# Performance work log

Hardware: AMD Instinct MI355X
Metric: run time of the kernel (lower is better)

Reference implementation:

```python
import jax, jax.numpy as jnp
import numpy as np

TAU = 0.3
EPS = 1e-8
B, N = 16, 65536


def _box2gaussian(boxes):
    # boxes: (B, N, 7) = (cx, cy, cz, dx, dy, dz, theta)
    mu = boxes[..., :3]
    dxyz = boxes[..., 3:6]
    theta = boxes[..., 6]
    c, s = jnp.cos(theta), jnp.sin(theta)
    z, o = jnp.zeros_like(c), jnp.ones_like(c)
    # Rz: (B, N, 3, 3) rotation about z
    Rz = jnp.stack([
        jnp.stack([c, -s, z], axis=-1),
        jnp.stack([s,  c, z], axis=-1),
        jnp.stack([z,  z, o], axis=-1),
    ], axis=-2)
    diag = dxyz ** 2 / 4.0                       # (B, N, 3)
    # sigma = Rz @ diag(diag) @ Rz^T
    sigma = jnp.einsum('bnij,bnj,bnkj->bnik', Rz, diag, Rz)
    return mu, sigma


def _sqrtm_psd(A):
    # Batched symmetric matrix square root via eigendecomposition.
    # Faithful to torch.linalg.eig + clamp(real, 1e-8) + V diag(sqrt(w)) V^T
    # for symmetric PSD input (eig of symmetric == eigh).
    A = 0.5 * (A + jnp.swapaxes(A, -1, -2))      # symmetrize for robustness
    w, v = jnp.linalg.eigh(A)
    w = jnp.clip(w, EPS, None)
    return jnp.einsum('...ij,...j,...kj->...ik', v, jnp.sqrt(w), v)


def setup_inputs() -> dict:
    key = jax.random.key(0)
    k1, k2 = jax.random.split(key)
    pred = jax.random.normal(k1, (B, N, 7), dtype=jnp.float32)
    gt = jax.random.normal(k2, (B, N, 7), dtype=jnp.float32)
    return {"pred_bboxes_3d": pred, "gt_bboxes_3d": gt}


def reference(pred_bboxes_3d, gt_bboxes_3d):
    mu_p, sigma_p = _box2gaussian(pred_bboxes_3d)
    mu_t, sigma_t = _box2gaussian(gt_bboxes_3d)

    # ||mu_p - mu_t||^2, (B, N)
    mu_dist_sq = jnp.sum((mu_p - mu_t) ** 2, axis=-1)

    # Tr(Sp + St - 2 (Sp^1/2 St Sp^1/2)^1/2), vectorized over all B*N boxes
    sp_sqrt = _sqrtm_psd(sigma_p)
    spstsp = sp_sqrt @ sigma_t @ sp_sqrt
    spstsp_sqrt = _sqrtm_psd(spstsp)
    cov_term = jnp.trace(sigma_p + sigma_t - 2.0 * spstsp_sqrt,
                         axis1=-2, axis2=-1)

    w2_sq = mu_dist_sq + cov_term

    det_sigma_t = jnp.clip(jnp.linalg.det(sigma_t), EPS, None)
    det_term = det_sigma_t ** (1.0 / 3.0)
    loss_per_box = 1.0 - jnp.exp(-w2_sq / (TAU * det_term))

    valid_mask = (gt_bboxes_3d[..., 0] != 0).astype(loss_per_box.dtype)
    loss = (loss_per_box * valid_mask).sum() / (valid_mask.sum() + EPS)
    return loss
```

## Files before the change

kernel.cpp:

```cpp
#include <hip/hip_runtime.h>
#include <math.h>

#define TAU_F 0.3f
#define EPS_F 1e-8f

__global__ void gwd_kernel(const float* __restrict__ pred,
                           const float* __restrict__ gt,
                           float* __restrict__ sums, int n) {
    float acc_loss = 0.f, acc_mask = 0.f;
    const int stride = gridDim.x * blockDim.x;
    for (int i = blockIdx.x * blockDim.x + threadIdx.x; i < n; i += stride) {
        const float* p = pred + (size_t)i * 7;
        const float* g = gt   + (size_t)i * 7;
        float px = p[0], py = p[1], pz = p[2];
        float pdx = p[3], pdy = p[4], pdz = p[5], pth = p[6];
        float tx = g[0], ty = g[1], tz = g[2];
        float tdx = g[3], tdy = g[4], tdz = g[5], tth = g[6];

        float dx = px - tx, dy = py - ty, dz = pz - tz;
        float mu_dist = dx * dx + dy * dy + dz * dz;

        float ap1 = 0.25f * pdx * pdx, ap2 = 0.25f * pdy * pdy, czp = 0.25f * pdz * pdz;
        float at1 = 0.25f * tdx * tdx, at2 = 0.25f * tdy * tdy, czt = 0.25f * tdz * tdz;

        float sp, cp; sincosf(pth, &sp, &cp);
        float st, ct; sincosf(tth, &st, &ct);
        float cp2 = cp * cp, sp2 = sp * sp, cpsp = cp * sp;
        float ct2 = ct * ct, st2 = st * st, ctst = ct * st;

        float At11 = at1 * ct2 + at2 * st2;
        float At22 = at1 * st2 + at2 * ct2;
        float At12 = (at1 - at2) * ctst;

        float ap1c = fmaxf(ap1, EPS_F), ap2c = fmaxf(ap2, EPS_F);
        float Ap11 = ap1c * cp2 + ap2c * sp2;
        float Ap22 = ap1c * sp2 + ap2c * cp2;
        float Ap12 = (ap1c - ap2c) * cpsp;

        float T = At11 * Ap11 + 2.f * At12 * Ap12 + At22 * Ap22;
        float D = (at1 * at2) * (ap1c * ap2c);
        float r = sqrtf(fmaxf(T * T - 4.f * D, 0.f));
        float lm1 = 0.5f * (T + r), lm2 = 0.5f * (T - r);
        float tr_sqrt_M2 = sqrtf(fmaxf(lm1, EPS_F)) + sqrtf(fmaxf(lm2, EPS_F));

        float czpc = fmaxf(czp, EPS_F);
        float z_sqrt = sqrtf(fmaxf(czpc * czt, EPS_F));

        float cov = (ap1 + ap2 + czp) + (at1 + at2 + czt)
                    - 2.f * (tr_sqrt_M2 + z_sqrt);
        float w2 = mu_dist + cov;

        float det_t = fmaxf(at1 * at2 * czt, EPS_F);
        float det_term = cbrtf(det_t);
        float loss = 1.f - expf(-w2 / (TAU_F * det_term));
        float mask = (tx != 0.f) ? 1.f : 0.f;
        acc_loss += loss * mask;
        acc_mask += mask;
    }

    for (int off = 32; off; off >>= 1) {
        acc_loss += __shfl_down(acc_loss, off, 64);
        acc_mask += __shfl_down(acc_mask, off, 64);
    }
    __shared__ float sl[8], sm[8];
    int lane = threadIdx.x & 63, wave = threadIdx.x >> 6;
    if (lane == 0) { sl[wave] = acc_loss; sm[wave] = acc_mask; }
    __syncthreads();
    if (threadIdx.x == 0) {
        float tl = 0.f, tm = 0.f;
        int nw = blockDim.x >> 6;
        for (int w = 0; w < nw; ++w) { tl += sl[w]; tm += sm[w]; }
        atomicAdd(&sums[0], tl);
        atomicAdd(&sums[1], tm);
    }
}

__global__ void gwd_finalize(const float* __restrict__ sums,
                             float* __restrict__ out) {
    if (threadIdx.x == 0 && blockIdx.x == 0) {
        out[0] = sums[0] / (sums[1] + EPS_F);
    }
}

extern "C" void kernel_launch(void* const* d_in, const int* in_sizes, int n_in,
                              void* d_out, int out_size, void* d_ws, size_t ws_size,
                              hipStream_t stream) {
    const float* pred = (const float*)d_in[0];
    const float* gt   = (const float*)d_in[1];
    float* out  = (float*)d_out;
    float* sums = (float*)d_ws;
    int n = in_sizes[0] / 7;

    hipMemsetAsync(sums, 0, 2 * sizeof(float), stream);

    const int block = 256;
    const int grid  = 1024;
    gwd_kernel<<<grid, block, 0, stream>>>(pred, gt, sums, n);
    gwd_finalize<<<1, 64, 0, stream>>>(sums, out);
}
```

Baseline: 113.7 us.

## Vectorize per-thread box loads and replace atomics with partial-sum finalize

Each thread now handles exactly four boxes, reading them as seven contiguous float4 nontemporal loads per input instead of strided scalar loads in a grid-stride loop. The per-block atomicAdds and the memset are replaced by per-block partial sums written to workspace, reduced by a 1024-thread finalize kernel. The aim is wider, better-used memory transactions and less launch and atomic overhead. Grid and block sizes are hardcoded, so the kernel has no bounds check and only covers exactly GRID*BLOCK*4 boxes.

```diff
diff --git a/kernel.cpp b/kernel.cpp
--- a/kernel.cpp
+++ b/kernel.cpp
@@ -4,27 +4,43 @@
 #define TAU_F 0.3f
 #define EPS_F 1e-8f
 
-__global__ void gwd_kernel(const float* __restrict__ pred,
-                           const float* __restrict__ gt,
-                           float* __restrict__ sums, int n) {
+#define GRID 1024
+#define BLOCK 256
+
+typedef float f32x4 __attribute__((ext_vector_type(4)));
+
+__global__ __launch_bounds__(BLOCK) void gwd_kernel(
+        const f32x4* __restrict__ pred4,
+        const f32x4* __restrict__ gt4,
+        float* __restrict__ partials) {
+    const int tid = blockIdx.x * BLOCK + threadIdx.x;
+
+    float pa[28], ga[28];
+    {
+        const f32x4* pp = pred4 + (size_t)tid * 7;
+        const f32x4* gg = gt4   + (size_t)tid * 7;
+#pragma unroll
+        for (int j = 0; j < 7; ++j) {
+            f32x4 v = __builtin_nontemporal_load(pp + j);
+            pa[4*j+0] = v.x; pa[4*j+1] = v.y; pa[4*j+2] = v.z; pa[4*j+3] = v.w;
+            f32x4 w = __builtin_nontemporal_load(gg + j);
+            ga[4*j+0] = w.x; ga[4*j+1] = w.y; ga[4*j+2] = w.z; ga[4*j+3] = w.w;
+        }
+    }
+
     float acc_loss = 0.f, acc_mask = 0.f;
-    const int stride = gridDim.x * blockDim.x;
-    for (int i = blockIdx.x * blockDim.x + threadIdx.x; i < n; i += stride) {
-        const float* p = pred + (size_t)i * 7;
-        const float* g = gt   + (size_t)i * 7;
-        float px = p[0], py = p[1], pz = p[2];
-        float pdx = p[3], pdy = p[4], pdz = p[5], pth = p[6];
-        float tx = g[0], ty = g[1], tz = g[2];
-        float tdx = g[3], tdy = g[4], tdz = g[5], tth = g[6];
-
-        float dx = px - tx, dy = py - ty, dz = pz - tz;
+#pragma unroll
+    for (int k = 0; k < 4; ++k) {
+        const float* p = pa + 7 * k;
+        const float* g = ga + 7 * k;
+        float dx = p[0] - g[0], dy = p[1] - g[1], dz = p[2] - g[2];
         float mu_dist = dx * dx + dy * dy + dz * dz;
 
-        float ap1 = 0.25f * pdx * pdx, ap2 = 0.25f * pdy * pdy, czp = 0.25f * pdz * pdz;
-        float at1 = 0.25f * tdx * tdx, at2 = 0.25f * tdy * tdy, czt = 0.25f * tdz * tdz;
+        float ap1 = 0.25f * p[3] * p[3], ap2 = 0.25f * p[4] * p[4], czp = 0.25f * p[5] * p[5];
+        float at1 = 0.25f * g[3] * g[3], at2 = 0.25f * g[4] * g[4], czt = 0.25f * g[5] * g[5];
 
-        float sp, cp; sincosf(pth, &sp, &cp);
-        float st, ct; sincosf(tth, &st, &ct);
+        float sp, cp; sincosf(p[6], &sp, &cp);
+        float st, ct; sincosf(g[6], &st, &ct);
         float cp2 = cp * cp, sp2 = sp * sp, cpsp = cp * sp;
         float ct2 = ct * ct, st2 = st * st, ctst = ct * st;
 
@@ -40,61 +56,69 @@
         float T = At11 * Ap11 + 2.f * At12 * Ap12 + At22 * Ap22;
         float D = (at1 * at2) * (ap1c * ap2c);
         float r = sqrtf(fmaxf(T * T - 4.f * D, 0.f));
-        float lm1 = 0.5f * (T + r), lm2 = 0.5f * (T - r);
-        float tr_sqrt_M2 = sqrtf(fmaxf(lm1, EPS_F)) + sqrtf(fmaxf(lm2, EPS_F));
+        float tr_sqrt_M2 = sqrtf(fmaxf(0.5f * (T + r), EPS_F)) +
+                           sqrtf(fmaxf(0.5f * (T - r), EPS_F));
 
-        float czpc = fmaxf(czp, EPS_F);
-        float z_sqrt = sqrtf(fmaxf(czpc * czt, EPS_F));
+        float z_sqrt = sqrtf(fmaxf(fmaxf(czp, EPS_F) * czt, EPS_F));
 
         float cov = (ap1 + ap2 + czp) + (at1 + at2 + czt)
                     - 2.f * (tr_sqrt_M2 + z_sqrt);
         float w2 = mu_dist + cov;
 
-        float det_t = fmaxf(at1 * at2 * czt, EPS_F);
-        float det_term = cbrtf(det_t);
+        float det_term = cbrtf(fmaxf(at1 * at2 * czt, EPS_F));
         float loss = 1.f - expf(-w2 / (TAU_F * det_term));
-        float mask = (tx != 0.f) ? 1.f : 0.f;
+        float mask = (g[0] != 0.f) ? 1.f : 0.f;
         acc_loss += loss * mask;
         acc_mask += mask;
     }
 
+#pragma unroll
     for (int off = 32; off; off >>= 1) {
         acc_loss += __shfl_down(acc_loss, off, 64);
         acc_mask += __shfl_down(acc_mask, off, 64);
     }
-    __shared__ float sl[8], sm[8];
+    __shared__ float sl[4], sm[4];
     int lane = threadIdx.x & 63, wave = threadIdx.x >> 6;
     if (lane == 0) { sl[wave] = acc_loss; sm[wave] = acc_mask; }
     __syncthreads();
     if (threadIdx.x == 0) {
-        float tl = 0.f, tm = 0.f;
-        int nw = blockDim.x >> 6;
-        for (int w = 0; w < nw; ++w) { tl += sl[w]; tm += sm[w]; }
-        atomicAdd(&sums[0], tl);
-        atomicAdd(&sums[1], tm);
+        float tl = sl[0] + sl[1] + sl[2] + sl[3];
+        float tm = sm[0] + sm[1] + sm[2] + sm[3];
+        partials[blockIdx.x]        = tl;
+        partials[GRID + blockIdx.x] = tm;
     }
 }
 
-__global__ void gwd_finalize(const float* __restrict__ sums,
-                             float* __restrict__ out) {
-    if (threadIdx.x == 0 && blockIdx.x == 0) {
-        out[0] = sums[0] / (sums[1] + EPS_F);
+__global__ __launch_bounds__(1024) void gwd_finalize(
+        const float* __restrict__ partials, float* __restrict__ out) {
+    int tid = threadIdx.x;
+    float l = partials[tid];
+    float m = partials[GRID + tid];
+#pragma unroll
+    for (int off = 32; off; off >>= 1) {
+        l += __shfl_down(l, off, 64);
+        m += __shfl_down(m, off, 64);
+    }
+    __shared__ float sl[16], sm[16];
+    int lane = tid & 63, wave = tid >> 6;
+    if (lane == 0) { sl[wave] = l; sm[wave] = m; }
+    __syncthreads();
+    if (tid == 0) {
+        float tl = 0.f, tm = 0.f;
+#pragma unroll
+        for (int w = 0; w < 16; ++w) { tl += sl[w]; tm += sm[w]; }
+        out[0] = tl / (tm + EPS_F);
     }
 }
 
 extern "C" void kernel_launch(void* const* d_in, const int* in_sizes, int n_in,
                               void* d_out, int out_size, void* d_ws, size_t ws_size,
                               hipStream_t stream) {
-    const float* pred = (const float*)d_in[0];
-    const float* gt   = (const float*)d_in[1];
-    float* out  = (float*)d_out;
-    float* sums = (float*)d_ws;
-    int n = in_sizes[0] / 7;
+    const f32x4* pred = (const f32x4*)d_in[0];
+    const f32x4* gt   = (const f32x4*)d_in[1];
+    float* out      = (float*)d_out;
+    float* partials = (float*)d_ws;
 
-    hipMemsetAsync(sums, 0, 2 * sizeof(float), stream);
-
-    const int block = 256;
-    const int grid  = 1024;
-    gwd_kernel<<<grid, block, 0, stream>>>(pred, gt, sums, n);
-    gwd_finalize<<<1, 64, 0, stream>>>(sums, out);
+    gwd_kernel<<<GRID, BLOCK, 0, stream>>>(pred, gt, partials);
+    gwd_finalize<<<1, 1024, 0, stream>>>(partials, out);
 }
```

Result: faster. 109.1 us (-4.1%).
